# Performance work log

Measured on AMD Instinct MI355X. Metric: run time of the kernel, lower is better.

## Reference

```python
import jax, jax.numpy as jnp
from jax import lax
import numpy as np

N_ATOMS = 4096
ATOM_SIZE = 8
CHANNELS = 64
BATCH = 4
FRAMES = 256


def setup_inputs() -> dict:
    key = jax.random.key(0)
    k1, k2 = jax.random.split(key)
    x = jax.random.normal(k1, (BATCH, CHANNELS, FRAMES), dtype=jnp.float32)
    # dictionary parameter, uniform(-1, 1) as in nn.Parameter(...).uniform_(-1, 1)
    d = jax.random.uniform(k2, (N_ATOMS, CHANNELS, ATOM_SIZE), dtype=jnp.float32, minval=-1.0, maxval=1.0)
    return {"x": x, "d": d, "n_iterations": 32}


def _unit_norm(d):
    # normalize each atom over (channels, atom_size), dims (-1, -2)
    n = jnp.linalg.norm(d.reshape(d.shape[0], -1), axis=-1)
    return d / (n[:, None, None] + 1e-8)


def reference(x, d, n_iterations):
    B, C, T = x.shape
    n_atoms, _, atom_size = d.shape
    dn = _unit_norm(d)
    # pad residual on the right so atoms placed near the end fit entirely
    pad = atom_size
    res0 = jnp.pad(x, ((0, 0), (0, 0), (0, pad)))          # [B, C, T+pad]
    recon0 = jnp.zeros_like(res0)
    P = T + pad - atom_size + 1                             # valid correlation positions

    def step(carry, _):
        res, recon = carry
        # correlate residual with every (unit-norm) atom: [B, n_atoms, P]
        fm = lax.conv_general_dilated(
            res, dn, window_strides=(1,), padding='VALID',
            dimension_numbers=('NCH', 'OIH', 'NCH'))
        flat = fm.reshape(B, n_atoms * P)
        idx = jnp.argmax(flat, axis=-1)                     # top-1 per batch item
        atom_idx = idx // P
        pos = idx % P
        val = jnp.take_along_axis(flat, idx[:, None], axis=-1)[:, 0]
        atoms = dn[atom_idx] * val[:, None, None]           # [B, C, atom_size]

        def upd(r, rc, a, p):
            sl = lax.dynamic_slice(r, (0, p), (C, atom_size))
            r = lax.dynamic_update_slice(r, sl - a, (0, p))
            sr = lax.dynamic_slice(rc, (0, p), (C, atom_size))
            rc = lax.dynamic_update_slice(rc, sr + a, (0, p))
            return r, rc

        res, recon = jax.vmap(upd)(res, recon, atoms, pos)
        return (res, recon), None

    (res, recon), _ = lax.scan(step, (res0, recon0), None, length=n_iterations)
    return recon[..., :T]
```

## Files before the change

### kernel.cpp

```cpp
#include <hip/hip_runtime.h>

#define B 4
#define C 64
#define T 256
#define A 4096
#define RC 264
#define PW 260
#define NITER 32
#define NBLK 256
#define ATB 16
#define WSTR 44
#define WROW 2816

#define WS_DN     0
#define WS_RES    8388608
#define WS_RECON  8658944
#define WS_FM     8929280
#define WS_PARTS  25968640

typedef unsigned long long u64;

__device__ __forceinline__ u64 packmax21(float v, unsigned key) {
    unsigned u = __float_as_uint(v);
    u = (u & 0x80000000u) ? ~u : (u | 0x80000000u);
    return ((u64)u << 32) | ((u64)(0x1FFFFFu - key) << 11);
}
__device__ __forceinline__ void decode21(u64 m, int* atom, int* pos, float* val) {
    const unsigned key = 0x1FFFFFu - (unsigned)((m >> 11) & 0x1FFFFFu);
    unsigned uv = (unsigned)(m >> 32);
    uv = (uv & 0x80000000u) ? (uv & 0x7FFFFFFFu) : ~uv;
    *atom = (int)(key / PW); *pos = (int)(key % PW); *val = __uint_as_float(uv);
}

__global__ void k_norm(const float* __restrict__ d, float* __restrict__ dn) {
    const int atom = blockIdx.x * 4 + (threadIdx.x >> 6);
    const int lane = threadIdx.x & 63;
    const float* src = d + atom * 512;
    float4 v0 = ((const float4*)src)[lane * 2];
    float4 v1 = ((const float4*)src)[lane * 2 + 1];
    float s = v0.x*v0.x + v0.y*v0.y + v0.z*v0.z + v0.w*v0.w
            + v1.x*v1.x + v1.y*v1.y + v1.z*v1.z + v1.w*v1.w;
    #pragma unroll
    for (int off = 32; off; off >>= 1) s += __shfl_xor(s, off);
    const float denom = sqrtf(s) + 1e-8f;
    float* dst = dn + atom * 512;
    float4 o0 = make_float4(v0.x/denom, v0.y/denom, v0.z/denom, v0.w/denom);
    float4 o1 = make_float4(v1.x/denom, v1.y/denom, v1.z/denom, v1.w/denom);
    ((float4*)dst)[lane * 2]     = o0;
    ((float4*)dst)[lane * 2 + 1] = o1;
}

__global__ void k_init(const float* __restrict__ x, float* __restrict__ res,
                       float* __restrict__ recon, float* __restrict__ fm) {
    const int tid = blockIdx.x * blockDim.x + threadIdx.x;
    const int nth = gridDim.x * blockDim.x;
    for (int i = tid; i < B * C * RC; i += nth) {
        const int col = i % RC;
        const int bc  = i / RC;
        res[i]   = (col < T) ? x[bc * T + col] : 0.0f;
        recon[i] = 0.0f;
    }
    for (int i = tid; i < B * A; i += nth) {
        float* row = fm + (long)i * PW;
        row[256] = 0.0f;
        row[257] = -1e30f; row[258] = -1e30f; row[259] = -1e30f;
    }
}

__global__ __launch_bounds__(256) void k_conv(const float* __restrict__ res,
                                              const float* __restrict__ dn,
                                              float* __restrict__ fm) {
    __shared__ __align__(16) float lr[16 * 264];
    __shared__ __align__(16) float ld[32 * 16 * 8];
    const int b  = blockIdx.y;
    const int a0 = blockIdx.x * 32;
    const int t  = threadIdx.x;
    const int slot = t >> 5;
    const int pg   = t & 31;
    const int p0   = pg * 8;

    float acc[4][8] = {};

    for (int cb = 0; cb < 4; ++cb) {
        const float* rsrc = res + b * C * RC + cb * 16 * RC;
        for (int i = t; i < 16 * 264; i += 256) lr[i] = rsrc[i];
        const float* dsrc = dn + (long)a0 * 512 + cb * 128;
        for (int i = t; i < 4096; i += 256)
            ld[i] = dsrc[(long)(i >> 7) * 512 + (i & 127)];
        __syncthreads();

        for (int cc = 0; cc < 16; ++cc) {
            float rv[16];
            const float* r = lr + cc * 264 + p0;
            *(float4*)(rv)      = *(const float4*)(r);
            *(float4*)(rv + 4)  = *(const float4*)(r + 4);
            *(float4*)(rv + 8)  = *(const float4*)(r + 8);
            *(float4*)(rv + 12) = *(const float4*)(r + 12);
            float dk[32];
            #pragma unroll
            for (int ai = 0; ai < 4; ++ai) {
                const float* dp = ld + ((slot * 4 + ai) * 16 + cc) * 8;
                *(float4*)(dk + ai * 8)     = *(const float4*)(dp);
                *(float4*)(dk + ai * 8 + 4) = *(const float4*)(dp + 4);
            }
            #pragma unroll
            for (int ai = 0; ai < 4; ++ai)
                #pragma unroll
                for (int pi = 0; pi < 8; ++pi)
                    #pragma unroll
                    for (int kk = 0; kk < 8; ++kk)
                        acc[ai][pi] = fmaf(rv[pi + kk], dk[ai * 8 + kk], acc[ai][pi]);
        }
        __syncthreads();
    }

    #pragma unroll
    for (int ai = 0; ai < 4; ++ai) {
        float* outp = fm + ((long)b * A + a0 + slot * 4 + ai) * PW + p0;
        *(float4*)(outp)     = *(const float4*)&acc[ai][0];
        *(float4*)(outp + 4) = *(const float4*)&acc[ai][4];
    }
}

__global__ __launch_bounds__(512) void k_scan0(const float* __restrict__ fm,
                                               u64* __restrict__ rmax_g,
                                               u64* __restrict__ parts0) {
    __shared__ u64 rmax[4][ATB];
    const int bk = blockIdx.x, a0 = bk * ATB, t = threadIdx.x;
    const int wv = t >> 6, ln = t & 63;
    const int row = t >> 3, kk8 = t & 7, r_ai = row & 15, r_b = row >> 4;
    const float* frow = fm + ((long)r_b * A + a0 + r_ai) * PW;
    const unsigned rkey = (unsigned)((a0 + r_ai) * PW);

    u64 m = 0ull;
    #pragma unroll
    for (int i = 0; i <= 8; ++i) {
        const int idx4 = kk8 + i * 8;
        if (idx4 < 65) {
            const float4 v = ((const float4*)frow)[idx4];
            const unsigned e = rkey + idx4 * 4;
            u64 q0 = packmax21(v.x, e);
            u64 q1 = packmax21(v.y, e + 1);
            u64 q2 = packmax21(v.z, e + 2);
            u64 q3 = packmax21(v.w, e + 3);
            if (q1 > q0) q0 = q1;
            if (q3 > q2) q2 = q3;
            if (q2 > q0) q0 = q2;
            if (q0 > m)  m = q0;
        }
    }
    #pragma unroll
    for (int off = 1; off <= 4; off <<= 1) {
        u64 o = __shfl_xor(m, off);
        if (o > m) m = o;
    }
    if (kk8 == 0) {
        rmax[r_b][r_ai] = m;
        rmax_g[(size_t)r_b * A + a0 + r_ai] = m;
    }
    __syncthreads();
    if (wv == 0) {
        const int b_ = ln >> 4, ai_ = ln & 15;
        u64 mm = rmax[b_][ai_];
        #pragma unroll
        for (int off = 1; off <= 8; off <<= 1) {
            u64 o = __shfl_xor(mm, off);
            if (o > mm) mm = o;
        }
        if (ai_ == 0) parts0[b_ * 256 + bk] = mm;
    }
}

__global__ __launch_bounds__(512) void k_step(const float* __restrict__ dn,
                                              float* __restrict__ recon,
                                              float* __restrict__ fm,
                                              u64* __restrict__ rmax_g,
                                              const u64* __restrict__ pin,
                                              u64* __restrict__ pout) {
    __shared__ __align__(16) float wpad[4][WROW];
    __shared__ float g[ATB][4][17];
    __shared__ u64 rmax[4][ATB];
    __shared__ int sflag[64];
    __shared__ int   watom[4], wpos[4];
    __shared__ float wval[4];

    const int bk = blockIdx.x, a0 = bk * ATB, t = threadIdx.x;
    const int wv = t >> 6, ln = t & 63;
    const int a_ = t >> 5, tt = t & 31, bb_ = tt & 3, cg = tt >> 2;
    const int row = t >> 3, kk8 = t & 7, r_ai = row & 15, r_b = row >> 4;
    float* frow = fm + ((long)r_b * A + a0 + r_ai) * PW;
    const unsigned rkey = (unsigned)((a0 + r_ai) * PW);

    float own[8][8];
    {
        const float* s = dn + (long)(a0 + a_) * 512 + cg * 8;
        #pragma unroll
        for (int j = 0; j < 8; ++j) {
            *(float4*)&own[j][0] = *(const float4*)(s + j * 64);
            *(float4*)&own[j][4] = *(const float4*)(s + j * 64 + 4);
        }
    }
    for (int i = t; i < 4 * WROW; i += 512) ((float*)wpad)[i] = 0.0f;

    if (wv < 4) {
        const u64* pb = pin + wv * 256 + ln * 4;
        u64 m0 = pb[0], m1 = pb[1], m2 = pb[2], m3 = pb[3];
        if (m1 > m0) m0 = m1;
        if (m3 > m2) m2 = m3;
        if (m2 > m0) m0 = m2;
        #pragma unroll
        for (int off = 1; off <= 32; off <<= 1) {
            u64 o = __shfl_xor(m0, off);
            if (o > m0) m0 = o;
        }
        if (ln == 0) decode21(m0, &watom[wv], &wpos[wv], &wval[wv]);
    } else if (wv == 4) {
        rmax[ln >> 4][ln & 15] = rmax_g[(size_t)(ln >> 4) * A + a0 + (ln & 15)];
    }
    __syncthreads();

    if (bk >= 4 && bk < 8) {
        const int b = bk - 4;
        const float cv = wval[b];
        const float* dw = dn + (long)watom[b] * 512;
        recon[(long)(b * C + (t >> 3)) * RC + wpos[b] + (t & 7)] += cv * dw[t];
    }

    for (int i = t; i < 4 * 512; i += 512) {
        const int b = i >> 9, r = i & 511;
        wpad[b][(r >> 3) * WSTR + 8 + (r & 7)] = dn[(long)watom[b] * 512 + r];
    }
    __syncthreads();

    {
        float acc[15];
        #pragma unroll
        for (int i = 0; i < 15; ++i) acc[i] = 0.0f;
        #pragma unroll
        for (int j = 0; j < 8; ++j) {
            const float* wp = &wpad[bb_][(j * 8 + cg) * WSTR];
            float wr[24];
            *(float4*)(wr)      = *(const float4*)(wp);
            *(float4*)(wr + 4)  = *(const float4*)(wp + 4);
            *(float4*)(wr + 8)  = *(const float4*)(wp + 8);
            *(float4*)(wr + 12) = *(const float4*)(wp + 12);
            *(float4*)(wr + 16) = *(const float4*)(wp + 16);
            *(float4*)(wr + 20) = *(const float4*)(wp + 20);
            #pragma unroll
            for (int di = 0; di < 15; ++di)
                #pragma unroll
                for (int k = 0; k < 8; ++k)
                    acc[di] = fmaf(own[j][k], wr[15 + k - di], acc[di]);
        }
        #pragma unroll
        for (int di = 0; di < 15; ++di) {
            acc[di] += __shfl_xor(acc[di], 4);
            acc[di] += __shfl_xor(acc[di], 8);
            acc[di] += __shfl_xor(acc[di], 16);
        }
        if (cg == 0) {
            #pragma unroll
            for (int di = 0; di < 15; ++di) g[a_][bb_][di] = acc[di];
        }
    }
    __syncthreads();

    {
        const int q = wpos[r_b];
        const float val = wval[r_b];
        u64 wm = 0ull;
        #pragma unroll
        for (int h = 0; h < 2; ++h) {
            const int di = kk8 + h * 8;
            if (di < 15) {
                const int p = q + 7 - di;
                if (p >= 0 && p <= 256) {
                    const float nv = frow[p] - val * g[r_ai][r_b][di];
                    frow[p] = nv;
                    const u64 pm = packmax21(nv, rkey + p);
                    if (pm > wm) wm = pm;
                }
            }
        }
        #pragma unroll
        for (int off = 1; off <= 4; off <<= 1) {
            u64 o = __shfl_xor(wm, off);
            if (o > wm) wm = o;
        }
        if (kk8 == 0) {
            const u64 old = rmax[r_b][r_ai];
            const unsigned okey = 0x1FFFFFu - (unsigned)((old >> 11) & 0x1FFFFFu);
            const int opos = (int)(okey % PW);
            if (opos >= q - 7 && opos <= q + 7) {
                sflag[row] = 1;
            } else {
                sflag[row] = 0;
                rmax[r_b][r_ai] = (old > wm) ? old : wm;
            }
        }
    }
    __syncthreads();

    if (sflag[row]) {
        u64 m = 0ull;
        #pragma unroll
        for (int i = 0; i <= 8; ++i) {
            const int idx4 = kk8 + i * 8;
            if (idx4 < 65) {
                const float4 v = ((const float4*)frow)[idx4];
                const unsigned e = rkey + idx4 * 4;
                u64 q0 = packmax21(v.x, e);
                u64 q1 = packmax21(v.y, e + 1);
                u64 q2 = packmax21(v.z, e + 2);
                u64 q3 = packmax21(v.w, e + 3);
                if (q1 > q0) q0 = q1;
                if (q3 > q2) q2 = q3;
                if (q2 > q0) q0 = q2;
                if (q0 > m)  m = q0;
            }
        }
        #pragma unroll
        for (int off = 1; off <= 4; off <<= 1) {
            u64 o = __shfl_xor(m, off);
            if (o > m) m = o;
        }
        if (kk8 == 0) rmax[r_b][r_ai] = m;
    }
    __syncthreads();

    if (wv == 0) {
        const int b_ = ln >> 4, ai_ = ln & 15;
        u64 m = rmax[b_][ai_];
        #pragma unroll
        for (int off = 1; off <= 8; off <<= 1) {
            u64 o = __shfl_xor(m, off);
            if (o > m) m = o;
        }
        if (ai_ == 0) pout[b_ * 256 + bk] = m;
    } else if (wv == 1) {
        rmax_g[(size_t)(ln >> 4) * A + a0 + (ln & 15)] = rmax[ln >> 4][ln & 15];
    }
}

__global__ __launch_bounds__(512) void k_last(const float* __restrict__ dn,
                                              float* __restrict__ recon,
                                              const u64* __restrict__ pin,
                                              float* __restrict__ out) {
    __shared__ int s_atom, s_pos;
    __shared__ float s_val;
    const int b = blockIdx.x, t = threadIdx.x;
    const int wv = t >> 6, ln = t & 63;
    if (wv == 0) {
        const u64* pb = pin + b * 256 + ln * 4;
        u64 m0 = pb[0], m1 = pb[1], m2 = pb[2], m3 = pb[3];
        if (m1 > m0) m0 = m1;
        if (m3 > m2) m2 = m3;
        if (m2 > m0) m0 = m2;
        #pragma unroll
        for (int off = 1; off <= 32; off <<= 1) {
            u64 o = __shfl_xor(m0, off);
            if (o > m0) m0 = o;
        }
        if (ln == 0) decode21(m0, &s_atom, &s_pos, &s_val);
    }
    __syncthreads();
    recon[(long)(b * C + (t >> 3)) * RC + s_pos + (t & 7)] += s_val * dn[(long)s_atom * 512 + t];
    __syncthreads();
    for (int i = t; i < C * T / 4; i += 512) {
        const int c = i >> 6, t4 = i & 63;
        ((float4*)out)[b * 4096 + i] = *(const float4*)&recon[(long)(b * C + c) * RC + t4 * 4];
    }
}

extern "C" void kernel_launch(void* const* d_in, const int* in_sizes, int n_in,
                              void* d_out, int out_size, void* d_ws, size_t ws_size,
                              hipStream_t stream) {
    const float* x = (const float*)d_in[0];
    const float* d = (const float*)d_in[1];
    char* ws = (char*)d_ws;
    float* dn     = (float*)(ws + WS_DN);
    float* res    = (float*)(ws + WS_RES);
    u64*   rmax_g = (u64*)(ws + WS_RES);
    float* recon  = (float*)(ws + WS_RECON);
    float* fm     = (float*)(ws + WS_FM);
    u64*   parts  = (u64*)(ws + WS_PARTS);
    float* out    = (float*)d_out;
    u64* p0 = parts;
    u64* p1 = parts + 1024;

    hipLaunchKernelGGL(k_norm, dim3(A / 4), dim3(256), 0, stream, d, dn);
    hipLaunchKernelGGL(k_init, dim3(1024), dim3(256), 0, stream, x, res, recon, fm);
    hipLaunchKernelGGL(k_conv, dim3(A / 32, B), dim3(256), 0, stream, res, dn, fm);
    hipLaunchKernelGGL(k_scan0, dim3(NBLK), dim3(512), 0, stream, fm, rmax_g, p0);

    for (int it = 0; it < NITER - 1; ++it) {
        u64* pi = (it & 1) ? p1 : p0;
        u64* po = (it & 1) ? p0 : p1;
        hipLaunchKernelGGL(k_step, dim3(NBLK), dim3(512), 0, stream,
                           dn, recon, fm, rmax_g, pi, po);
    }
    hipLaunchKernelGGL(k_last, dim3(B), dim3(512), 0, stream, dn, recon, p1, out);
}
```

Measured before the change: 548.8 us.

## Fuse normalization into init and argmax scan into conv; swizzle LDS, widen tiles

Folds the dictionary normalization into the init kernel and the first argmax scan into the conv kernel's epilogue. This removes two launches and a full re-read of the feature map. The conv kernel drops to 128 threads, each computing 16 positions, and uses an XOR swizzle on the shared-memory tiles to reduce bank conflicts. rmax_g moves out of the res buffer to its own workspace region. Costs are higher register pressure and lower per-block parallelism in conv.

```diff
diff --git a/kernel.cpp b/kernel.cpp
--- a/kernel.cpp
+++ b/kernel.cpp
@@ -17,8 +17,11 @@
 #define WS_RECON  8658944
 #define WS_FM     8929280
 #define WS_PARTS  25968640
+#define WS_RMAX   25985024
 
 typedef unsigned long long u64;
+
+#define SW(w) ((w) ^ ((((w) >> 5) & 7) << 2))
 
 __device__ __forceinline__ u64 packmax21(float v, unsigned key) {
     unsigned u = __float_as_uint(v);
@@ -32,27 +35,28 @@
     *atom = (int)(key / PW); *pos = (int)(key % PW); *val = __uint_as_float(uv);
 }
 
-__global__ void k_norm(const float* __restrict__ d, float* __restrict__ dn) {
-    const int atom = blockIdx.x * 4 + (threadIdx.x >> 6);
-    const int lane = threadIdx.x & 63;
-    const float* src = d + atom * 512;
-    float4 v0 = ((const float4*)src)[lane * 2];
-    float4 v1 = ((const float4*)src)[lane * 2 + 1];
-    float s = v0.x*v0.x + v0.y*v0.y + v0.z*v0.z + v0.w*v0.w
-            + v1.x*v1.x + v1.y*v1.y + v1.z*v1.z + v1.w*v1.w;
-    #pragma unroll
-    for (int off = 32; off; off >>= 1) s += __shfl_xor(s, off);
-    const float denom = sqrtf(s) + 1e-8f;
-    float* dst = dn + atom * 512;
-    float4 o0 = make_float4(v0.x/denom, v0.y/denom, v0.z/denom, v0.w/denom);
-    float4 o1 = make_float4(v1.x/denom, v1.y/denom, v1.z/denom, v1.w/denom);
-    ((float4*)dst)[lane * 2]     = o0;
-    ((float4*)dst)[lane * 2 + 1] = o1;
-}
-
-__global__ void k_init(const float* __restrict__ x, float* __restrict__ res,
+__global__ void k_init(const float* __restrict__ x, const float* __restrict__ d,
+                       float* __restrict__ dn, float* __restrict__ res,
                        float* __restrict__ recon, float* __restrict__ fm) {
-    const int tid = blockIdx.x * blockDim.x + threadIdx.x;
+    const int t = threadIdx.x;
+    {
+        const int atom = blockIdx.x * 4 + (t >> 6);
+        const int lane = t & 63;
+        const float* src = d + atom * 512;
+        float4 v0 = ((const float4*)src)[lane * 2];
+        float4 v1 = ((const float4*)src)[lane * 2 + 1];
+        float s = v0.x*v0.x + v0.y*v0.y + v0.z*v0.z + v0.w*v0.w
+                + v1.x*v1.x + v1.y*v1.y + v1.z*v1.z + v1.w*v1.w;
+        #pragma unroll
+        for (int off = 32; off; off >>= 1) s += __shfl_xor(s, off);
+        const float denom = sqrtf(s) + 1e-8f;
+        float* dst = dn + atom * 512;
+        float4 o0 = make_float4(v0.x/denom, v0.y/denom, v0.z/denom, v0.w/denom);
+        float4 o1 = make_float4(v1.x/denom, v1.y/denom, v1.z/denom, v1.w/denom);
+        ((float4*)dst)[lane * 2]     = o0;
+        ((float4*)dst)[lane * 2 + 1] = o1;
+    }
+    const int tid = blockIdx.x * blockDim.x + t;
     const int nth = gridDim.x * blockDim.x;
     for (int i = tid; i < B * C * RC; i += nth) {
         const int col = i % RC;
@@ -67,107 +71,97 @@
     }
 }
 
-__global__ __launch_bounds__(256) void k_conv(const float* __restrict__ res,
+__global__ __launch_bounds__(128) void k_conv(const float* __restrict__ res,
                                               const float* __restrict__ dn,
-                                              float* __restrict__ fm) {
+                                              float* __restrict__ fm,
+                                              u64* __restrict__ rmax_g,
+                                              u64* __restrict__ parts0) {
     __shared__ __align__(16) float lr[16 * 264];
     __shared__ __align__(16) float ld[32 * 16 * 8];
+    __shared__ u64 rr[32];
+    const int ck = blockIdx.x;
     const int b  = blockIdx.y;
-    const int a0 = blockIdx.x * 32;
+    const int a0 = ck * 32;
     const int t  = threadIdx.x;
-    const int slot = t >> 5;
-    const int pg   = t & 31;
-    const int p0   = pg * 8;
-
-    float acc[4][8] = {};
+    const int slot = t >> 4;
+    const int pg   = t & 15;
+    const int p0   = pg * 16;
+
+    float acc[4][16] = {};
 
     for (int cb = 0; cb < 4; ++cb) {
-        const float* rsrc = res + b * C * RC + cb * 16 * RC;
-        for (int i = t; i < 16 * 264; i += 256) lr[i] = rsrc[i];
+        const float* rsrc = res + (b * C + cb * 16) * RC;
+        for (int i = t; i < 16 * 264; i += 128) lr[SW(i)] = rsrc[i];
         const float* dsrc = dn + (long)a0 * 512 + cb * 128;
-        for (int i = t; i < 4096; i += 256)
-            ld[i] = dsrc[(long)(i >> 7) * 512 + (i & 127)];
+        for (int i = t; i < 4096; i += 128)
+            ld[SW(i)] = dsrc[(long)(i >> 7) * 512 + (i & 127)];
         __syncthreads();
 
         for (int cc = 0; cc < 16; ++cc) {
-            float rv[16];
-            const float* r = lr + cc * 264 + p0;
-            *(float4*)(rv)      = *(const float4*)(r);
-            *(float4*)(rv + 4)  = *(const float4*)(r + 4);
-            *(float4*)(rv + 8)  = *(const float4*)(r + 8);
-            *(float4*)(rv + 12) = *(const float4*)(r + 12);
-            float dk[32];
+            float rv[24];
+            const int base = cc * 264 + p0;
+            #pragma unroll
+            for (int j = 0; j < 6; ++j)
+                *(float4*)(rv + 4 * j) = *(const float4*)&lr[SW(base + 4 * j)];
             #pragma unroll
             for (int ai = 0; ai < 4; ++ai) {
-                const float* dp = ld + ((slot * 4 + ai) * 16 + cc) * 8;
-                *(float4*)(dk + ai * 8)     = *(const float4*)(dp);
-                *(float4*)(dk + ai * 8 + 4) = *(const float4*)(dp + 4);
-            }
-            #pragma unroll
-            for (int ai = 0; ai < 4; ++ai)
+                const int dbase = ((slot * 4 + ai) * 16 + cc) * 8;
+                float dk[8];
+                *(float4*)(dk)     = *(const float4*)&ld[SW(dbase)];
+                *(float4*)(dk + 4) = *(const float4*)&ld[SW(dbase + 4)];
                 #pragma unroll
-                for (int pi = 0; pi < 8; ++pi)
+                for (int pi = 0; pi < 16; ++pi)
                     #pragma unroll
                     for (int kk = 0; kk < 8; ++kk)
-                        acc[ai][pi] = fmaf(rv[pi + kk], dk[ai * 8 + kk], acc[ai][pi]);
+                        acc[ai][pi] = fmaf(rv[pi + kk], dk[kk], acc[ai][pi]);
+            }
         }
         __syncthreads();
     }
 
+    u64 pm[4];
     #pragma unroll
     for (int ai = 0; ai < 4; ++ai) {
-        float* outp = fm + ((long)b * A + a0 + slot * 4 + ai) * PW + p0;
-        *(float4*)(outp)     = *(const float4*)&acc[ai][0];
-        *(float4*)(outp + 4) = *(const float4*)&acc[ai][4];
-    }
-}
-
-__global__ __launch_bounds__(512) void k_scan0(const float* __restrict__ fm,
-                                               u64* __restrict__ rmax_g,
-                                               u64* __restrict__ parts0) {
-    __shared__ u64 rmax[4][ATB];
-    const int bk = blockIdx.x, a0 = bk * ATB, t = threadIdx.x;
-    const int wv = t >> 6, ln = t & 63;
-    const int row = t >> 3, kk8 = t & 7, r_ai = row & 15, r_b = row >> 4;
-    const float* frow = fm + ((long)r_b * A + a0 + r_ai) * PW;
-    const unsigned rkey = (unsigned)((a0 + r_ai) * PW);
-
-    u64 m = 0ull;
+        const int row = a0 + slot * 4 + ai;
+        float* outp = fm + ((long)b * A + row) * PW + p0;
+        *(float4*)(outp)      = *(const float4*)&acc[ai][0];
+        *(float4*)(outp + 4)  = *(const float4*)&acc[ai][4];
+        *(float4*)(outp + 8)  = *(const float4*)&acc[ai][8];
+        *(float4*)(outp + 12) = *(const float4*)&acc[ai][12];
+        const unsigned rkey = (unsigned)(row * PW);
+        u64 m = 0ull;
+        #pragma unroll
+        for (int i = 0; i < 16; ++i) {
+            const u64 q = packmax21(acc[ai][i], rkey + p0 + i);
+            if (q > m) m = q;
+        }
+        pm[ai] = m;
+    }
     #pragma unroll
-    for (int i = 0; i <= 8; ++i) {
-        const int idx4 = kk8 + i * 8;
-        if (idx4 < 65) {
-            const float4 v = ((const float4*)frow)[idx4];
-            const unsigned e = rkey + idx4 * 4;
-            u64 q0 = packmax21(v.x, e);
-            u64 q1 = packmax21(v.y, e + 1);
-            u64 q2 = packmax21(v.z, e + 2);
-            u64 q3 = packmax21(v.w, e + 3);
-            if (q1 > q0) q0 = q1;
-            if (q3 > q2) q2 = q3;
-            if (q2 > q0) q0 = q2;
-            if (q0 > m)  m = q0;
-        }
-    }
-    #pragma unroll
-    for (int off = 1; off <= 4; off <<= 1) {
-        u64 o = __shfl_xor(m, off);
-        if (o > m) m = o;
-    }
-    if (kk8 == 0) {
-        rmax[r_b][r_ai] = m;
-        rmax_g[(size_t)r_b * A + a0 + r_ai] = m;
-    }
-    __syncthreads();
-    if (wv == 0) {
-        const int b_ = ln >> 4, ai_ = ln & 15;
-        u64 mm = rmax[b_][ai_];
-        #pragma unroll
-        for (int off = 1; off <= 8; off <<= 1) {
-            u64 o = __shfl_xor(mm, off);
-            if (o > mm) mm = o;
-        }
-        if (ai_ == 0) parts0[b_ * 256 + bk] = mm;
+    for (int off = 1; off <= 8; off <<= 1) {
+        #pragma unroll
+        for (int ai = 0; ai < 4; ++ai) {
+            u64 o = __shfl_xor(pm[ai], off);
+            if (o > pm[ai]) pm[ai] = o;
+        }
+    }
+    if (pg == 0) {
+        #pragma unroll
+        for (int ai = 0; ai < 4; ++ai) {
+            const int row = a0 + slot * 4 + ai;
+            u64 m = pm[ai];
+            const u64 z = packmax21(0.0f, (unsigned)(row * PW) + 256);
+            if (z > m) m = z;
+            rmax_g[(size_t)b * A + row] = m;
+            rr[slot * 4 + ai] = m;
+        }
+    }
+    __syncthreads();
+    if (t < 2) {
+        u64 m = rr[t * 16];
+        #pragma unroll
+        for (int i = 1; i < 16; ++i) if (rr[t * 16 + i] > m) m = rr[t * 16 + i];
+        parts0[b * 256 + ck * 2 + t] = m;
     }
 }
 
@@ -380,18 +374,16 @@
     char* ws = (char*)d_ws;
     float* dn     = (float*)(ws + WS_DN);
     float* res    = (float*)(ws + WS_RES);
-    u64*   rmax_g = (u64*)(ws + WS_RES);
     float* recon  = (float*)(ws + WS_RECON);
     float* fm     = (float*)(ws + WS_FM);
     u64*   parts  = (u64*)(ws + WS_PARTS);
+    u64*   rmax_g = (u64*)(ws + WS_RMAX);
     float* out    = (float*)d_out;
     u64* p0 = parts;
     u64* p1 = parts + 1024;
 
-    hipLaunchKernelGGL(k_norm, dim3(A / 4), dim3(256), 0, stream, d, dn);
-    hipLaunchKernelGGL(k_init, dim3(1024), dim3(256), 0, stream, x, res, recon, fm);
-    hipLaunchKernelGGL(k_conv, dim3(A / 32, B), dim3(256), 0, stream, res, dn, fm);
-    hipLaunchKernelGGL(k_scan0, dim3(NBLK), dim3(512), 0, stream, fm, rmax_g, p0);
+    hipLaunchKernelGGL(k_init, dim3(1024), dim3(256), 0, stream, x, d, dn, res, recon, fm);
+    hipLaunchKernelGGL(k_conv, dim3(A / 32, B), dim3(128), 0, stream, res, dn, fm, rmax_g, p0);
 
     for (int it = 0; it < NITER - 1; ++it) {
         u64* pi = (it & 1) ? p1 : p0;
```

Measured after the change: 563.2 us. 1.03x slower.
